# Optimization experiments

Hardware: AMD Instinct MI355X
Metric: run time of the kernel (lower is better)

## Reference

```python
import jax, jax.numpy as jnp
import numpy as np

N, D, H, E, K = 65536, 128, 256, 32, 2


def setup_inputs() -> dict:
    key = jax.random.key(0)
    ks = jax.random.split(key, 7)
    s_in = 1.0 / np.sqrt(D)
    s_hid = 1.0 / np.sqrt(H)
    return {
        "x": jax.random.normal(ks[0], (N, D), dtype=jnp.float32),
        "W1": jax.random.uniform(ks[1], (E, D, H), jnp.float32, -s_in, s_in),
        "b1": jax.random.uniform(ks[2], (E, H), jnp.float32, -s_in, s_in),
        "W2": jax.random.uniform(ks[3], (E, H, D), jnp.float32, -s_hid, s_hid),
        "b2": jax.random.uniform(ks[4], (E, D), jnp.float32, -s_hid, s_hid),
        "Wr": jax.random.uniform(ks[5], (D, E), jnp.float32, -s_in, s_in),
        "br": jax.random.uniform(ks[6], (E,), jnp.float32, -s_in, s_in),
    }


def reference(x, W1, b1, W2, b2, Wr, br):
    # Router (eval mode: no gate noise)
    logits = x @ Wr + br                                  # [N, E]
    scores = jax.nn.softmax(logits, axis=-1)              # [N, E]
    topk_vals, topk_inds = jax.lax.top_k(scores, K)       # [N, K]

    # dispatch_mask: zeros scattered with top-k probs (scatter_ on dim 1)
    n = x.shape[0]
    dispatch_mask = jnp.zeros_like(scores).at[
        jnp.arange(n)[:, None], topk_inds
    ].set(topk_vals)                                      # [N, E]

    # Dense all-experts compute, as in the reference torch.stack
    h = jax.nn.relu(jnp.einsum("nd,edh->neh", x, W1) + b1)   # [N, E, H]
    expert_outputs = jnp.einsum("neh,ehd->ned", h, W2) + b2  # [N, E, D]

    output = jnp.einsum("ned,ne->nd", expert_outputs, dispatch_mask)  # [N, D]

    importance = dispatch_mask.sum(axis=0)                # [E]
    imp_mean = jnp.mean(importance)
    imp_var = jnp.var(importance, ddof=1)                 # torch.var is unbiased
    load_balancing_loss = imp_var / (imp_mean ** 2 + 1e-9)
    return output, load_balancing_loss
```

## Files before the change

### kernel.cpp

```cpp
#include <hip/hip_runtime.h>
#include <hip/hip_bf16.h>
#include <cstdint>
#include <cstddef>

#define N_TOK 65536
#define DIM 128
#define HID 256
#define NE 32
#define TOPK 2

typedef __bf16 bf16x8 __attribute__((ext_vector_type(8)));
typedef float f32x4 __attribute__((ext_vector_type(4)));
typedef unsigned uint4v __attribute__((ext_vector_type(4)));

#define LDSA(c, row, byte) ((((c) * 1024 + (row) * 16 + (byte))) ^ ((((c) & 3) << 5)))

__device__ __forceinline__ unsigned short f2bf(float f) {
  unsigned u = __builtin_bit_cast(unsigned, f);
  u += 0x7fffu + ((u >> 16) & 1u);
  return (unsigned short)(u >> 16);
}
__device__ __forceinline__ float bf2f(unsigned s) {
  return __builtin_bit_cast(float, s << 16);
}
__device__ __forceinline__ uint2 split2(float f0, float f1) {
  unsigned u0 = __builtin_bit_cast(unsigned, f0);
  unsigned u1 = __builtin_bit_cast(unsigned, f1);
  unsigned hi = (u0 >> 16) | (u1 & 0xffff0000u);
  float r0 = f0 - __builtin_bit_cast(float, u0 & 0xffff0000u);
  float r1 = f1 - __builtin_bit_cast(float, u1 & 0xffff0000u);
  unsigned lo = (__builtin_bit_cast(unsigned, r0) >> 16) |
                (__builtin_bit_cast(unsigned, r1) & 0xffff0000u);
  uint2 ret; ret.x = hi; ret.y = lo;
  return ret;
}

__global__ void k_zero_out(float* __restrict__ out) {
  int t = blockIdx.x * 256 + threadIdx.x;
  float4 z = make_float4(0.f, 0.f, 0.f, 0.f);
  float4* o4 = (float4*)out;
  o4[t] = z;
  o4[t + 1048576] = z;
}

__global__ __launch_bounds__(256, 2) void k_front(
    const float* __restrict__ x, const float* __restrict__ W1,
    const float* __restrict__ W2, const float* __restrict__ Wr,
    const float* __restrict__ br,
    int* __restrict__ top_idx, float* __restrict__ top_val,
    unsigned short* __restrict__ xb,
    unsigned short* __restrict__ w1t, unsigned short* __restrict__ w2t,
    int* __restrict__ histbuf, float* __restrict__ impbuf) {
  int b = blockIdx.x;
  int t = threadIdx.x;

  if (b >= 512) {
    int bb = b - 512;
    const float* in;
    unsigned short* outp;
    int K, r0, c0;
    bool isW1;
    if (bb < 256) {
      int e = bb >> 3, tt = bb & 7;
      in = W1 + (size_t)e * DIM * HID;
      outp = w1t + (size_t)e * DIM * HID;
      K = HID;
      r0 = (tt >> 2) * 64; c0 = (tt & 3) * 64;
      isW1 = true;
    } else {
      bb -= 256;
      int e = bb >> 3, tt = bb & 7;
      in = W2 + (size_t)e * HID * DIM;
      outp = w2t + (size_t)e * HID * DIM;
      K = DIM;
      r0 = (tt >> 1) * 64; c0 = (tt & 1) * 64;
      isW1 = false;
    }
    __shared__ float tile[64][65];
    int r = t >> 2, cs = (t & 3) * 16;
    const float* src = in + (size_t)(r0 + r) * K + c0 + cs;
#pragma unroll
    for (int j = 0; j < 4; ++j) {
      float4 v = *(const float4*)(src + j * 4);
      tile[r][cs + j * 4 + 0] = v.x;
      tile[r][cs + j * 4 + 1] = v.y;
      tile[r][cs + j * 4 + 2] = v.z;
      tile[r][cs + j * 4 + 3] = v.w;
    }
    __syncthreads();
#pragma unroll
    for (int p = 0; p < 2; ++p) {
      int orow = p * 32 + (t >> 3);
      int oc8 = (t & 7) * 8;
      int rr = r0 + oc8;
      unsigned pk[4];
#pragma unroll
      for (int q = 0; q < 4; ++q) {
        unsigned lo = f2bf(tile[oc8 + 2 * q][orow]);
        unsigned hi = f2bf(tile[oc8 + 2 * q + 1][orow]);
        pk[q] = lo | (hi << 16);
      }
      uint4 u;
      u.x = pk[0]; u.y = pk[1]; u.z = pk[2]; u.w = pk[3];
      int h = c0 + orow;
      int hp = isW1 ? ((h & ~63) | ((h & 3) << 4) | ((h & 63) >> 2))
                    : ((h & ~31) | ((h & 1) << 4) | ((h & 31) >> 1));
      size_t addr = (size_t)(rr >> 5) * (K * 32) + (size_t)hp * 32 + (rr & 31);
      *(uint4*)(outp + addr) = u;
    }
    return;
  }

  __shared__ int hc[NE];
  __shared__ float hf[NE];
  __shared__ int slist[128];
  __shared__ int scount;
  if (t < NE) { hc[t] = 0; hf[t] = 0.f; }
  if (t == 0) scount = 0;
  __syncthreads();

  int w = t >> 6, l = t & 63, quad = l >> 4, l15 = l & 15;
  int tok0 = b * 128 + w * 32;

  bf16x8 bfr[2][2][4];
#pragma unroll
  for (int nt = 0; nt < 2; ++nt)
#pragma unroll
    for (int kc = 0; kc < 4; ++kc) {
      unsigned hiw[4], low[4];
#pragma unroll
      for (int jp = 0; jp < 4; ++jp) {
        int k0 = kc * 32 + quad * 8 + jp * 2;
        int e = nt * 16 + l15;
        float w0 = Wr[k0 * NE + e];
        float w1v = Wr[(k0 + 1) * NE + e];
        uint2 s = split2(w0, w1v);
        hiw[jp] = s.x; low[jp] = s.y;
      }
      uint4v h4, l4;
      h4[0] = hiw[0]; h4[1] = hiw[1]; h4[2] = hiw[2]; h4[3] = hiw[3];
      l4[0] = low[0]; l4[1] = low[1]; l4[2] = low[2]; l4[3] = low[3];
      bfr[0][nt][kc] = __builtin_bit_cast(bf16x8, h4);
      bfr[1][nt][kc] = __builtin_bit_cast(bf16x8, l4);
    }

  f32x4 acc[2][2];
#pragma unroll
  for (int a = 0; a < 2; ++a)
#pragma unroll
    for (int bb = 0; bb < 2; ++bb) {
      f32x4 z = {0.f, 0.f, 0.f, 0.f};
      acc[a][bb] = z;
    }

#pragma unroll
  for (int mt = 0; mt < 2; ++mt) {
    const float* xp = x + (size_t)(tok0 + mt * 16 + l15) * DIM + quad * 8;
    float4 va[4][2];
#pragma unroll
    for (int kc = 0; kc < 4; ++kc) {
      const float4* p = (const float4*)(xp + kc * 32);
      va[kc][0] = p[0];
      va[kc][1] = p[1];
    }
    unsigned short* xrow = xb + (size_t)(tok0 + mt * 16 + l15) * DIM + quad * 8;
#pragma unroll
    for (int kc = 0; kc < 4; ++kc) {
      uint4 u;
      u.x = (unsigned)f2bf(va[kc][0].x) | ((unsigned)f2bf(va[kc][0].y) << 16);
      u.y = (unsigned)f2bf(va[kc][0].z) | ((unsigned)f2bf(va[kc][0].w) << 16);
      u.z = (unsigned)f2bf(va[kc][1].x) | ((unsigned)f2bf(va[kc][1].y) << 16);
      u.w = (unsigned)f2bf(va[kc][1].z) | ((unsigned)f2bf(va[kc][1].w) << 16);
      *(uint4*)(xrow + kc * 32) = u;
    }
#pragma unroll
    for (int kc = 0; kc < 4; ++kc) {
      uint2 s0 = split2(va[kc][0].x, va[kc][0].y);
      uint2 s1 = split2(va[kc][0].z, va[kc][0].w);
      uint2 s2 = split2(va[kc][1].x, va[kc][1].y);
      uint2 s3 = split2(va[kc][1].z, va[kc][1].w);
      uint4v hu, lu;
      hu[0] = s0.x; lu[0] = s0.y;
      hu[1] = s1.x; lu[1] = s1.y;
      hu[2] = s2.x; lu[2] = s2.y;
      hu[3] = s3.x; lu[3] = s3.y;
      bf16x8 ahi = __builtin_bit_cast(bf16x8, hu);
      bf16x8 alo = __builtin_bit_cast(bf16x8, lu);
#pragma unroll
      for (int nt = 0; nt < 2; ++nt) {
        acc[mt][nt] = __builtin_amdgcn_mfma_f32_16x16x32_bf16(ahi, bfr[0][nt][kc], acc[mt][nt], 0, 0, 0);
        acc[mt][nt] = __builtin_amdgcn_mfma_f32_16x16x32_bf16(ahi, bfr[1][nt][kc], acc[mt][nt], 0, 0, 0);
        acc[mt][nt] = __builtin_amdgcn_mfma_f32_16x16x32_bf16(alo, bfr[0][nt][kc], acc[mt][nt], 0, 0, 0);
      }
    }
  }

  float brv0 = br[l15], brv1 = br[16 + l15];
  const float NINF = -3.0e38f;
#pragma unroll
  for (int mt = 0; mt < 2; ++mt) {
#pragma unroll
    for (int r = 0; r < 4; ++r) {
      float c0 = acc[mt][0][r] + brv0;
      float c1 = acc[mt][1][r] + brv1;
      float va = (c0 >= c1) ? c0 : c1;
      int ia = (c0 >= c1) ? l15 : 16 + l15;
#pragma unroll
      for (int off = 1; off < 16; off <<= 1) {
        float ov = __shfl_xor(va, off);
        int oi = __shfl_xor(ia, off);
        if (ov > va || (ov == va && oi < ia)) { va = ov; ia = oi; }
      }
      float v1 = va; int i1 = ia;
      float d0 = (i1 == l15) ? NINF : c0;
      float d1 = (i1 == 16 + l15) ? NINF : c1;
      float vb = (d0 >= d1) ? d0 : d1;
      int ib = (d0 >= d1) ? l15 : 16 + l15;
#pragma unroll
      for (int off = 1; off < 16; off <<= 1) {
        float ov = __shfl_xor(vb, off);
        int oi = __shfl_xor(ib, off);
        if (ov > vb || (ov == vb && oi < ib)) { vb = ov; ib = oi; }
      }
      float v2 = vb; int i2 = ib;
      float e0 = (i1 == l15 || i2 == l15) ? NINF : c0;
      float e1 = (i1 == 16 + l15 || i2 == 16 + l15) ? NINF : c1;
      float vc = (e0 >= e1) ? e0 : e1;
#pragma unroll
      for (int off = 1; off < 16; off <<= 1) {
        float ov = __shfl_xor(vc, off);
        vc = (ov > vc) ? ov : vc;
      }
      float s = __expf(c0 - v1) + __expf(c1 - v1);
#pragma unroll
      for (int off = 1; off < 16; off <<= 1) s += __shfl_xor(s, off);
      if (l15 == 0) {
        int n = tok0 + mt * 16 + quad * 4 + r;
        int2 ti; ti.x = i1; ti.y = i2;
        float2 tv; tv.x = 1.0f / s; tv.y = __expf(v2 - v1) / s;
        ((int2*)top_idx)[n] = ti;
        ((float2*)top_val)[n] = tv;
        atomicAdd(&hc[i1], 1);
        atomicAdd(&hc[i2], 1);
        atomicAdd(&hf[i1], tv.x);
        atomicAdd(&hf[i2], tv.y);
        if (v2 - vc < 2e-3f) {
          int si = atomicAdd(&scount, 1);
          if (si < 128) slist[si] = n;
        }
      }
    }
  }
  __syncthreads();

  int sc = scount;
  for (int s = (t >> 5); s < sc; s += 8) {
    int lt = t & 31;
    int n = slist[s];
    const float* xr = x + (size_t)n * DIM;
    double a = 0.0;
#pragma unroll 8
    for (int d = 0; d < DIM; ++d) a = fma((double)xr[d], (double)Wr[d * NE + lt], a);
    double lv = a + (double)br[lt];

    double v1 = lv; int i1 = lt;
#pragma unroll
    for (int off = 16; off > 0; off >>= 1) {
      double ov = __shfl_xor(v1, off, 32);
      int oi = __shfl_xor(i1, off, 32);
      if (ov > v1 || (ov == v1 && oi < i1)) { v1 = ov; i1 = oi; }
    }
    double lv2 = (lt == i1) ? -1.0e300 : lv;
    double v2 = lv2; int i2 = lt;
#pragma unroll
    for (int off = 16; off > 0; off >>= 1) {
      double ov = __shfl_xor(v2, off, 32);
      int oi = __shfl_xor(i2, off, 32);
      if (ov > v2 || (ov == v2 && oi < i2)) { v2 = ov; i2 = oi; }
    }
    float p = expf((float)(lv - v1));
    float ssum = p;
#pragma unroll
    for (int off = 16; off > 0; off >>= 1) ssum += __shfl_xor(ssum, off, 32);
    if (lt == 0) {
      int o1 = top_idx[n * 2 + 0];
      int o2 = top_idx[n * 2 + 1];
      float w1v = top_val[n * 2 + 0];
      float w2v = top_val[n * 2 + 1];
      float nv1 = 1.0f / ssum;
      float nv2 = expf((float)(v2 - v1)) / ssum;
      atomicAdd(&hc[o1], -1); atomicAdd(&hc[o2], -1);
      atomicAdd(&hc[i1], 1);  atomicAdd(&hc[i2], 1);
      atomicAdd(&hf[o1], -w1v); atomicAdd(&hf[o2], -w2v);
      atomicAdd(&hf[i1], nv1);  atomicAdd(&hf[i2], nv2);
      top_idx[n * 2 + 0] = i1;
      top_idx[n * 2 + 1] = i2;
      top_val[n * 2 + 0] = nv1;
      top_val[n * 2 + 1] = nv2;
    }
  }
  __syncthreads();
  if (t < NE) {
    histbuf[b * NE + t] = hc[t];
    impbuf[b * NE + t] = hf[t];
  }
}

__global__ __launch_bounds__(256) void k_scatter2(
    const int* __restrict__ top_idx, const float* __restrict__ top_val,
    const int* __restrict__ histbuf, const float* __restrict__ impbuf,
    int* __restrict__ perm, float* __restrict__ gatev, int* __restrict__ inv,
    int* __restrict__ offsets, int* __restrict__ counts, float* __restrict__ out_loss) {
  __shared__ int pf[8][32], pb[8][32];
  __shared__ int offs[NE], pref[NE], h2[NE];
  int b = blockIdx.x, t = threadIdx.x;
  if (t < NE) h2[t] = 0;
  int g = t >> 5, e = t & 31;
  int sf = 0, sb = 0;
  for (int j = 0; j < 64; ++j) {
    int bb = g * 64 + j;
    int v = histbuf[bb * NE + e];
    sf += v;
    sb += (bb < b) ? v : 0;
  }
  pf[g][e] = sf;
  pb[g][e] = sb;
  __syncthreads();
  if (t < 32) {
    int T = 0, P = 0;
#pragma unroll
    for (int g2 = 0; g2 < 8; ++g2) { T += pf[g2][t]; P += pb[g2][t]; }
    int pc = (T + 63) & ~63;
    int scn = pc;
#pragma unroll
    for (int off = 1; off < 32; off <<= 1) {
      int ov = __shfl_up(scn, off, 32);
      if (t >= off) scn += ov;
    }
    offs[t] = scn - pc;
    pref[t] = P;
    if (b == 0) {
      offsets[t] = scn - pc;
      counts[t] = T;
      if (t == 31) offsets[NE] = scn;
    }
  }
  __syncthreads();
  if (t < 128) {
    int n = b * 128 + t;
    int2 ti = ((const int2*)top_idx)[n];
    float2 tv = ((const float2*)top_val)[n];
    int r0 = atomicAdd(&h2[ti.x], 1);
    int r1 = atomicAdd(&h2[ti.y], 1);
    int p0 = offs[ti.x] + pref[ti.x] + r0;
    int p1 = offs[ti.y] + pref[ti.y] + r1;
    perm[p0] = n;
    gatev[p0] = tv.x;
    perm[p1] = n;
    gatev[p1] = tv.y;
    int2 iv; iv.x = p0; iv.y = p1;
    ((int2*)inv)[n] = iv;
  }
  if (b == 0) {
    __shared__ float pfi[8][32];
    float s2 = 0.f;
    for (int j = 0; j < 64; ++j) s2 += impbuf[(g * 64 + j) * NE + e];
    pfi[g][e] = s2;
    __syncthreads();
    if (t < 32) {
      float imp = 0.f;
#pragma unroll
      for (int g2 = 0; g2 < 8; ++g2) imp += pfi[g2][t];
      float ssum = imp;
#pragma unroll
      for (int off = 16; off > 0; off >>= 1) ssum += __shfl_xor(ssum, off, 32);
      float mean = ssum / 32.0f;
      float dlt = imp - mean;
      float v = dlt * dlt;
#pragma unroll
      for (int off = 16; off > 0; off >>= 1) v += __shfl_xor(v, off, 32);
      if (t == 0) *out_loss = (v / 31.0f) / (mean * mean + 1e-9f);
    }
  }
}

template <int YB>
__global__ __launch_bounds__(256, 3) void k_expert(
    const float* __restrict__ x, const unsigned short* __restrict__ xb,
    const unsigned short* __restrict__ w1t, const unsigned short* __restrict__ w2t,
    const float* __restrict__ b1, const float* __restrict__ b2,
    const int* __restrict__ offsets, const int* __restrict__ counts,
    const int* __restrict__ perm, const float* __restrict__ gatev,
    unsigned short* __restrict__ ybuf, float* __restrict__ out) {
  __shared__ __align__(16) unsigned char smem[32768];

  int bid = (int)(blockIdx.x & 7) * 260 + (int)(blockIdx.x >> 3);
  int slot0 = bid * 64;
  if (slot0 >= offsets[NE]) return;
  int e = 0;
#pragma unroll
  for (int i = 1; i < NE; ++i)
    if (slot0 >= offsets[i]) e = i;
  int cnt = counts[e];
  int local0 = slot0 - offsets[e];
  int nvalid = min(64, cnt - local0);

  int t = threadIdx.x;
  int w = t >> 6;
  int l = t & 63;
  int quad = l >> 4;
  int l15 = l & 15;

  int pvl = 0;
  float gvl = 0.f;
  if (YB) {
    uint4 v[4];
    if (l < nvalid) {
      pvl = perm[slot0 + l];
      gvl = gatev[slot0 + l];
      const uint4* rowp = (const uint4*)(xb + (size_t)pvl * DIM);
#pragma unroll
      for (int cc = 0; cc < 4; ++cc) v[cc] = rowp[w * 4 + cc];
    } else {
#pragma unroll
      for (int cc = 0; cc < 4; ++cc) { v[cc].x = 0u; v[cc].y = 0u; v[cc].z = 0u; v[cc].w = 0u; }
    }
#pragma unroll
    for (int cc = 0; cc < 4; ++cc)
      *(uint4*)(smem + LDSA(w * 4 + cc, l, 0)) = v[cc];
  } else {
    unsigned pk[16];
    if (l < nvalid) {
      pvl = perm[slot0 + l];
      gvl = gatev[slot0 + l];
      const float* src = x + (size_t)pvl * DIM + w * 32;
#pragma unroll
      for (int q = 0; q < 8; ++q) {
        float4 vv = ((const float4*)src)[q];
        pk[q * 2 + 0] = (unsigned)f2bf(vv.x) | ((unsigned)f2bf(vv.y) << 16);
        pk[q * 2 + 1] = (unsigned)f2bf(vv.z) | ((unsigned)f2bf(vv.w) << 16);
      }
    } else {
#pragma unroll
      for (int q = 0; q < 16; ++q) pk[q] = 0u;
    }
#pragma unroll
    for (int cc = 0; cc < 4; ++cc) {
      uint4 u;
      u.x = pk[cc * 4 + 0]; u.y = pk[cc * 4 + 1]; u.z = pk[cc * 4 + 2]; u.w = pk[cc * 4 + 3];
      *(uint4*)(smem + LDSA(w * 4 + cc, l, 0)) = u;
    }
  }

  const unsigned short* w1e = w1t + (size_t)e * DIM * HID;
  bf16x8 w1f[4][4];
#pragma unroll
  for (int kc = 0; kc < 4; ++kc)
#pragma unroll
    for (int jt = 0; jt < 4; ++jt)
      w1f[kc][jt] = *(const bf16x8*)(w1e + kc * 8192 + (w * 64 + jt * 16 + l15) * 32 + quad * 8);

  __syncthreads();

  f32x4 acc[4][4];
#pragma unroll
  for (int a = 0; a < 4; ++a)
#pragma unroll
    for (int bb = 0; bb < 4; ++bb) {
      f32x4 z = {0.f, 0.f, 0.f, 0.f};
      acc[a][bb] = z;
    }
#pragma unroll
  for (int kc = 0; kc < 4; ++kc) {
    bf16x8 af[4];
#pragma unroll
    for (int rt = 0; rt < 4; ++rt)
      af[rt] = *(const bf16x8*)(smem + LDSA(kc * 4 + quad, rt * 16 + l15, 0));
#pragma unroll
    for (int rt = 0; rt < 4; ++rt)
#pragma unroll
      for (int jt = 0; jt < 4; ++jt)
        acc[rt][jt] = __builtin_amdgcn_mfma_f32_16x16x32_bf16(af[rt], w1f[kc][jt], acc[rt][jt], 0, 0, 0);
  }

  const unsigned short* w2e = w2t + (size_t)e * HID * DIM;
  bf16x8 w2f[8][2];
#pragma unroll
  for (int hc = 0; hc < 8; ++hc)
#pragma unroll
    for (int jt = 0; jt < 2; ++jt)
      w2f[hc][jt] = *(const bf16x8*)(w2e + hc * 4096 + (w * 32 + jt * 16 + l15) * 32 + quad * 8);

  __syncthreads();

  {
    float4 b1v = *(const float4*)(b1 + e * HID + w * 64 + 4 * l15);
    int c = w * 8 + (l15 >> 1);
    int byte = (l15 & 1) * 8;
#pragma unroll
    for (int rt = 0; rt < 4; ++rt) {
#pragma unroll
      for (int r = 0; r < 4; ++r) {
        int tokrow = rt * 16 + quad * 4 + r;
        float v0 = acc[rt][0][r] + b1v.x; v0 = v0 > 0.f ? v0 : 0.f;
        float v1 = acc[rt][1][r] + b1v.y; v1 = v1 > 0.f ? v1 : 0.f;
        float v2 = acc[rt][2][r] + b1v.z; v2 = v2 > 0.f ? v2 : 0.f;
        float v3 = acc[rt][3][r] + b1v.w; v3 = v3 > 0.f ? v3 : 0.f;
        uint2 u;
        u.x = (unsigned)f2bf(v0) | ((unsigned)f2bf(v1) << 16);
        u.y = (unsigned)f2bf(v2) | ((unsigned)f2bf(v3) << 16);
        *(uint2*)(smem + LDSA(c, tokrow, byte)) = u;
      }
    }
  }
  __syncthreads();

  f32x4 accc[4][2];
#pragma unroll
  for (int a = 0; a < 4; ++a)
#pragma unroll
    for (int bb = 0; bb < 2; ++bb) {
      f32x4 z = {0.f, 0.f, 0.f, 0.f};
      accc[a][bb] = z;
    }
#pragma unroll
  for (int hc = 0; hc < 8; ++hc) {
    bf16x8 ah[4];
#pragma unroll
    for (int rt = 0; rt < 4; ++rt)
      ah[rt] = *(const bf16x8*)(smem + LDSA(hc * 4 + quad, rt * 16 + l15, 0));
#pragma unroll
    for (int rt = 0; rt < 4; ++rt)
#pragma unroll
      for (int jt = 0; jt < 2; ++jt)
        accc[rt][jt] = __builtin_amdgcn_mfma_f32_16x16x32_bf16(ah[rt], w2f[hc][jt], accc[rt][jt], 0, 0, 0);
  }

  int dbase = w * 32;
  float2 b2v = *(const float2*)(b2 + e * DIM + dbase + 2 * l15);
#pragma unroll
  for (int rt = 0; rt < 4; ++rt) {
#pragma unroll
    for (int r = 0; r < 4; ++r) {
      int tokrow = rt * 16 + quad * 4 + r;
      int pv = __shfl(pvl, tokrow);
      float g = __shfl(gvl, tokrow);
      if (tokrow < nvalid) {
        float y0 = g * (accc[rt][0][r] + b2v.x);
        float y1 = g * (accc[rt][1][r] + b2v.y);
        if (YB) {
          unsigned pack = (unsigned)f2bf(y0) | ((unsigned)f2bf(y1) << 16);
          *(unsigned*)(ybuf + (size_t)(slot0 + tokrow) * DIM + dbase + 2 * l15) = pack;
        } else {
          float* orow = out + (size_t)pv * DIM + dbase + 2 * l15;
          atomicAdd(&orow[0], y0);
          atomicAdd(&orow[1], y1);
        }
      }
    }
  }
}

__global__ __launch_bounds__(256) void k_combine(const unsigned short* __restrict__ ybuf,
                                                 const int* __restrict__ inv,
                                                 float* __restrict__ out) {
  int t = threadIdx.x;
  int n = blockIdx.x * 16 + (t >> 4);
  int lane = t & 15;
  int2 iv = ((const int2*)inv)[n];
  uint4 a = *((const uint4*)(ybuf + (size_t)iv.x * DIM) + lane);
  uint4 b = *((const uint4*)(ybuf + (size_t)iv.y * DIM) + lane);
  unsigned av[4] = {a.x, a.y, a.z, a.w}, bv[4] = {b.x, b.y, b.z, b.w};
  float r[8];
#pragma unroll
  for (int q = 0; q < 4; ++q) {
    r[q * 2 + 0] = bf2f(av[q] & 0xffffu) + bf2f(bv[q] & 0xffffu);
    r[q * 2 + 1] = bf2f(av[q] >> 16) + bf2f(bv[q] >> 16);
  }
  float* orow = out + (size_t)n * DIM + lane * 8;
  float4 w0 = {r[0], r[1], r[2], r[3]}, w1 = {r[4], r[5], r[6], r[7]};
  ((float4*)orow)[0] = w0;
  ((float4*)orow)[1] = w1;
}

extern "C" void kernel_launch(void* const* d_in, const int* in_sizes, int n_in,
                              void* d_out, int out_size, void* d_ws, size_t ws_size,
                              hipStream_t stream) {
  const float* x  = (const float*)d_in[0];
  const float* W1 = (const float*)d_in[1];
  const float* b1 = (const float*)d_in[2];
  const float* W2 = (const float*)d_in[3];
  const float* b2 = (const float*)d_in[4];
  const float* Wr = (const float*)d_in[5];
  const float* br = (const float*)d_in[6];
  float* out = (float*)d_out;

  char* ws = (char*)d_ws;
  int*   counts   = (int*)(ws + 0);
  int*   offsets  = (int*)(ws + 128);
  int*   top_idx  = (int*)(ws + 1024);
  float* top_val  = (float*)(ws + 525312);
  int*   perm     = (int*)(ws + 1049600);
  float* gatev    = (float*)(ws + 1582080);
  int*   inv      = (int*)(ws + 2114560);
  int*   histbuf  = (int*)(ws + 2638848);
  float* impbuf   = (float*)(ws + 2704384);
  unsigned short* w1t = (unsigned short*)(ws + 2769920);
  unsigned short* w2t = (unsigned short*)(ws + 4867072);
  unsigned short* ybuf = (unsigned short*)(ws + 6964224);
  const size_t NEEDED = 40518656;
  bool use_ybuf = ws_size >= NEEDED;

  unsigned short* xb = (unsigned short*)out;

  if (use_ybuf) {
    hipLaunchKernelGGL(k_front, dim3(1024), dim3(256), 0, stream, x, W1, W2, Wr, br,
                       top_idx, top_val, xb, w1t, w2t, histbuf, impbuf);
    hipLaunchKernelGGL(k_scatter2, dim3(512), dim3(256), 0, stream, top_idx, top_val,
                       histbuf, impbuf, perm, gatev, inv, offsets, counts,
                       out + (size_t)N_TOK * DIM);
    hipLaunchKernelGGL((k_expert<1>), dim3(2080), dim3(256), 0, stream, x, xb, w1t, w2t,
                       b1, b2, offsets, counts, perm, gatev, ybuf, out);
    hipLaunchKernelGGL(k_combine, dim3(4096), dim3(256), 0, stream, ybuf, inv, out);
  } else {
    hipLaunchKernelGGL(k_front, dim3(1024), dim3(256), 0, stream, x, W1, W2, Wr, br,
                       top_idx, top_val, xb, w1t, w2t, histbuf, impbuf);
    hipLaunchKernelGGL(k_scatter2, dim3(512), dim3(256), 0, stream, top_idx, top_val,
                       histbuf, impbuf, perm, gatev, inv, offsets, counts,
                       out + (size_t)N_TOK * DIM);
    hipLaunchKernelGGL(k_zero_out, dim3(4096), dim3(256), 0, stream, out);
    hipLaunchKernelGGL((k_expert<0>), dim3(2080), dim3(256), 0, stream, x,
                       (const unsigned short*)0, w1t, w2t, b1, b2, offsets, counts,
                       perm, gatev, (unsigned short*)0, out);
  }
}
```

Measured before the change: 178.0 us.

## Process two 64-token halves per expert block to reuse W1 fragments

Each expert block now handles 128 token slots as two 64-token halves. The W1 register fragments are loaded once and reused for both halves, and the second half's gather is issued early so it overlaps the first half's compute. W2 fragments are now streamed per hc iteration instead of held in registers, which frees registers but adds global loads inside the inner loop. Expert padding changes to 128, the grid halves, and the workspace is reordered so top_idx/top_val alias ybuf, adding extra padded rows and a longer serial chain per block.

```diff
diff --git a/kernel.cpp b/kernel.cpp
--- a/kernel.cpp
+++ b/kernel.cpp
@@ -330,7 +330,7 @@
     int T = 0, P = 0;
 #pragma unroll
     for (int g2 = 0; g2 < 8; ++g2) { T += pf[g2][t]; P += pb[g2][t]; }
-    int pc = (T + 63) & ~63;
+    int pc = (T + 127) & ~127;
     int scn = pc;
 #pragma unroll
     for (int off = 1; off < 32; off <<= 1) {
@@ -392,10 +392,11 @@
     const int* __restrict__ offsets, const int* __restrict__ counts,
     const int* __restrict__ perm, const float* __restrict__ gatev,
     unsigned short* __restrict__ ybuf, float* __restrict__ out) {
-  __shared__ __align__(16) unsigned char smem[32768];
-
-  int bid = (int)(blockIdx.x & 7) * 260 + (int)(blockIdx.x >> 3);
-  int slot0 = bid * 64;
+  __shared__ __align__(16) unsigned char xa[16384];
+  __shared__ __align__(16) unsigned char ha[32768];
+
+  int bid = (int)(blockIdx.x & 7) * 132 + (int)(blockIdx.x >> 3);
+  int slot0 = bid * 128;
   if (slot0 >= offsets[NE]) return;
   int e = 0;
 #pragma unroll
@@ -403,7 +404,9 @@
     if (slot0 >= offsets[i]) e = i;
   int cnt = counts[e];
   int local0 = slot0 - offsets[e];
-  int nvalid = min(64, cnt - local0);
+  int nvalid = min(128, cnt - local0);
+  int nv0 = nvalid < 64 ? nvalid : 64;
+  int nv1 = nvalid - nv0;
 
   int t = threadIdx.x;
   int w = t >> 6;
@@ -411,29 +414,40 @@
   int quad = l >> 4;
   int l15 = l & 15;
 
-  int pvl = 0;
-  float gvl = 0.f;
+  int pvl0 = 0, pvl1 = 0;
+  float gvl0 = 0.f, gvl1 = 0.f;
+  uint4 v1h[4];
   if (YB) {
-    uint4 v[4];
-    if (l < nvalid) {
-      pvl = perm[slot0 + l];
-      gvl = gatev[slot0 + l];
-      const uint4* rowp = (const uint4*)(xb + (size_t)pvl * DIM);
-#pragma unroll
-      for (int cc = 0; cc < 4; ++cc) v[cc] = rowp[w * 4 + cc];
+    uint4 v0[4];
+    if (l < nv0) {
+      pvl0 = perm[slot0 + l];
+      gvl0 = gatev[slot0 + l];
+      const uint4* rp = (const uint4*)(xb + (size_t)pvl0 * DIM);
+#pragma unroll
+      for (int cc = 0; cc < 4; ++cc) v0[cc] = rp[w * 4 + cc];
     } else {
 #pragma unroll
-      for (int cc = 0; cc < 4; ++cc) { v[cc].x = 0u; v[cc].y = 0u; v[cc].z = 0u; v[cc].w = 0u; }
+      for (int cc = 0; cc < 4; ++cc) { v0[cc].x = 0u; v0[cc].y = 0u; v0[cc].z = 0u; v0[cc].w = 0u; }
+    }
+    if (l < nv1) {
+      pvl1 = perm[slot0 + 64 + l];
+      gvl1 = gatev[slot0 + 64 + l];
+      const uint4* rp = (const uint4*)(xb + (size_t)pvl1 * DIM);
+#pragma unroll
+      for (int cc = 0; cc < 4; ++cc) v1h[cc] = rp[w * 4 + cc];
+    } else {
+#pragma unroll
+      for (int cc = 0; cc < 4; ++cc) { v1h[cc].x = 0u; v1h[cc].y = 0u; v1h[cc].z = 0u; v1h[cc].w = 0u; }
     }
 #pragma unroll
     for (int cc = 0; cc < 4; ++cc)
-      *(uint4*)(smem + LDSA(w * 4 + cc, l, 0)) = v[cc];
+      *(uint4*)(xa + LDSA(w * 4 + cc, l, 0)) = v0[cc];
   } else {
     unsigned pk[16];
-    if (l < nvalid) {
-      pvl = perm[slot0 + l];
-      gvl = gatev[slot0 + l];
-      const float* src = x + (size_t)pvl * DIM + w * 32;
+    if (l < nv0) {
+      pvl0 = perm[slot0 + l];
+      gvl0 = gatev[slot0 + l];
+      const float* src = x + (size_t)pvl0 * DIM + w * 32;
 #pragma unroll
       for (int q = 0; q < 8; ++q) {
         float4 vv = ((const float4*)src)[q];
@@ -444,11 +458,15 @@
 #pragma unroll
       for (int q = 0; q < 16; ++q) pk[q] = 0u;
     }
+    if (l < nv1) {
+      pvl1 = perm[slot0 + 64 + l];
+      gvl1 = gatev[slot0 + 64 + l];
+    }
 #pragma unroll
     for (int cc = 0; cc < 4; ++cc) {
       uint4 u;
       u.x = pk[cc * 4 + 0]; u.y = pk[cc * 4 + 1]; u.z = pk[cc * 4 + 2]; u.w = pk[cc * 4 + 3];
-      *(uint4*)(smem + LDSA(w * 4 + cc, l, 0)) = u;
+      *(uint4*)(xa + LDSA(w * 4 + cc, l, 0)) = u;
     }
   }
 
@@ -459,6 +477,11 @@
 #pragma unroll
     for (int jt = 0; jt < 4; ++jt)
       w1f[kc][jt] = *(const bf16x8*)(w1e + kc * 8192 + (w * 64 + jt * 16 + l15) * 32 + quad * 8);
+
+  const unsigned short* w2e = w2t + (size_t)e * HID * DIM;
+  float4 b1v = *(const float4*)(b1 + e * HID + w * 64 + 4 * l15);
+  int dbase = w * 32;
+  float2 b2v = *(const float2*)(b2 + e * DIM + dbase + 2 * l15);
 
   __syncthreads();
 
@@ -475,26 +498,42 @@
     bf16x8 af[4];
 #pragma unroll
     for (int rt = 0; rt < 4; ++rt)
-      af[rt] = *(const bf16x8*)(smem + LDSA(kc * 4 + quad, rt * 16 + l15, 0));
+      af[rt] = *(const bf16x8*)(xa + LDSA(kc * 4 + quad, rt * 16 + l15, 0));
 #pragma unroll
     for (int rt = 0; rt < 4; ++rt)
 #pragma unroll
       for (int jt = 0; jt < 4; ++jt)
         acc[rt][jt] = __builtin_amdgcn_mfma_f32_16x16x32_bf16(af[rt], w1f[kc][jt], acc[rt][jt], 0, 0, 0);
   }
-
-  const unsigned short* w2e = w2t + (size_t)e * HID * DIM;
-  bf16x8 w2f[8][2];
-#pragma unroll
-  for (int hc = 0; hc < 8; ++hc)
-#pragma unroll
-    for (int jt = 0; jt < 2; ++jt)
-      w2f[hc][jt] = *(const bf16x8*)(w2e + hc * 4096 + (w * 32 + jt * 16 + l15) * 32 + quad * 8);
-
-  __syncthreads();
+  __syncthreads();
+
+  if (YB) {
+#pragma unroll
+    for (int cc = 0; cc < 4; ++cc)
+      *(uint4*)(xa + LDSA(w * 4 + cc, l, 0)) = v1h[cc];
+  } else {
+    unsigned pk[16];
+    if (l < nv1) {
+      const float* src = x + (size_t)pvl1 * DIM + w * 32;
+#pragma unroll
+      for (int q = 0; q < 8; ++q) {
+        float4 vv = ((const float4*)src)[q];
+        pk[q * 2 + 0] = (unsigned)f2bf(vv.x) | ((unsigned)f2bf(vv.y) << 16);
+        pk[q * 2 + 1] = (unsigned)f2bf(vv.z) | ((unsigned)f2bf(vv.w) << 16);
+      }
+    } else {
+#pragma unroll
+      for (int q = 0; q < 16; ++q) pk[q] = 0u;
+    }
+#pragma unroll
+    for (int cc = 0; cc < 4; ++cc) {
+      uint4 u;
+      u.x = pk[cc * 4 + 0]; u.y = pk[cc * 4 + 1]; u.z = pk[cc * 4 + 2]; u.w = pk[cc * 4 + 3];
+      *(uint4*)(xa + LDSA(w * 4 + cc, l, 0)) = u;
+    }
+  }
 
   {
-    float4 b1v = *(const float4*)(b1 + e * HID + w * 64 + 4 * l15);
     int c = w * 8 + (l15 >> 1);
     int byte = (l15 & 1) * 8;
 #pragma unroll
@@ -509,7 +548,7 @@
         uint2 u;
         u.x = (unsigned)f2bf(v0) | ((unsigned)f2bf(v1) << 16);
         u.y = (unsigned)f2bf(v2) | ((unsigned)f2bf(v3) << 16);
-        *(uint2*)(smem + LDSA(c, tokrow, byte)) = u;
+        *(uint2*)(ha + LDSA(c, tokrow, byte)) = u;
       }
     }
   }
@@ -523,34 +562,118 @@
       f32x4 z = {0.f, 0.f, 0.f, 0.f};
       accc[a][bb] = z;
     }
-#pragma unroll
+#pragma unroll 2
   for (int hc = 0; hc < 8; ++hc) {
+    bf16x8 w2c0 = *(const bf16x8*)(w2e + hc * 4096 + (w * 32 + l15) * 32 + quad * 8);
+    bf16x8 w2c1 = *(const bf16x8*)(w2e + hc * 4096 + (w * 32 + 16 + l15) * 32 + quad * 8);
     bf16x8 ah[4];
 #pragma unroll
     for (int rt = 0; rt < 4; ++rt)
-      ah[rt] = *(const bf16x8*)(smem + LDSA(hc * 4 + quad, rt * 16 + l15, 0));
-#pragma unroll
-    for (int rt = 0; rt < 4; ++rt)
-#pragma unroll
-      for (int jt = 0; jt < 2; ++jt)
-        accc[rt][jt] = __builtin_amdgcn_mfma_f32_16x16x32_bf16(ah[rt], w2f[hc][jt], accc[rt][jt], 0, 0, 0);
-  }
-
-  int dbase = w * 32;
-  float2 b2v = *(const float2*)(b2 + e * DIM + dbase + 2 * l15);
+      ah[rt] = *(const bf16x8*)(ha + LDSA(hc * 4 + quad, rt * 16 + l15, 0));
+#pragma unroll
+    for (int rt = 0; rt < 4; ++rt) {
+      accc[rt][0] = __builtin_amdgcn_mfma_f32_16x16x32_bf16(ah[rt], w2c0, accc[rt][0], 0, 0, 0);
+      accc[rt][1] = __builtin_amdgcn_mfma_f32_16x16x32_bf16(ah[rt], w2c1, accc[rt][1], 0, 0, 0);
+    }
+  }
 #pragma unroll
   for (int rt = 0; rt < 4; ++rt) {
 #pragma unroll
     for (int r = 0; r < 4; ++r) {
       int tokrow = rt * 16 + quad * 4 + r;
-      int pv = __shfl(pvl, tokrow);
-      float g = __shfl(gvl, tokrow);
-      if (tokrow < nvalid) {
+      int pv = __shfl(pvl0, tokrow);
+      float g = __shfl(gvl0, tokrow);
+      if (tokrow < nv0) {
         float y0 = g * (accc[rt][0][r] + b2v.x);
         float y1 = g * (accc[rt][1][r] + b2v.y);
         if (YB) {
           unsigned pack = (unsigned)f2bf(y0) | ((unsigned)f2bf(y1) << 16);
           *(unsigned*)(ybuf + (size_t)(slot0 + tokrow) * DIM + dbase + 2 * l15) = pack;
+        } else {
+          float* orow = out + (size_t)pv * DIM + dbase + 2 * l15;
+          atomicAdd(&orow[0], y0);
+          atomicAdd(&orow[1], y1);
+        }
+      }
+    }
+  }
+
+#pragma unroll
+  for (int a = 0; a < 4; ++a)
+#pragma unroll
+    for (int bb = 0; bb < 4; ++bb) {
+      f32x4 z = {0.f, 0.f, 0.f, 0.f};
+      acc[a][bb] = z;
+    }
+#pragma unroll
+  for (int kc = 0; kc < 4; ++kc) {
+    bf16x8 af[4];
+#pragma unroll
+    for (int rt = 0; rt < 4; ++rt)
+      af[rt] = *(const bf16x8*)(xa + LDSA(kc * 4 + quad, rt * 16 + l15, 0));
+#pragma unroll
+    for (int rt = 0; rt < 4; ++rt)
+#pragma unroll
+      for (int jt = 0; jt < 4; ++jt)
+        acc[rt][jt] = __builtin_amdgcn_mfma_f32_16x16x32_bf16(af[rt], w1f[kc][jt], acc[rt][jt], 0, 0, 0);
+  }
+  __syncthreads();
+
+  {
+    int c = w * 8 + (l15 >> 1);
+    int byte = (l15 & 1) * 8;
+#pragma unroll
+    for (int rt = 0; rt < 4; ++rt) {
+#pragma unroll
+      for (int r = 0; r < 4; ++r) {
+        int tokrow = rt * 16 + quad * 4 + r;
+        float v0 = acc[rt][0][r] + b1v.x; v0 = v0 > 0.f ? v0 : 0.f;
+        float v1 = acc[rt][1][r] + b1v.y; v1 = v1 > 0.f ? v1 : 0.f;
+        float v2 = acc[rt][2][r] + b1v.z; v2 = v2 > 0.f ? v2 : 0.f;
+        float v3 = acc[rt][3][r] + b1v.w; v3 = v3 > 0.f ? v3 : 0.f;
+        uint2 u;
+        u.x = (unsigned)f2bf(v0) | ((unsigned)f2bf(v1) << 16);
+        u.y = (unsigned)f2bf(v2) | ((unsigned)f2bf(v3) << 16);
+        *(uint2*)(ha + LDSA(c, tokrow, byte)) = u;
+      }
+    }
+  }
+  __syncthreads();
+
+#pragma unroll
+  for (int a = 0; a < 4; ++a)
+#pragma unroll
+    for (int bb = 0; bb < 2; ++bb) {
+      f32x4 z = {0.f, 0.f, 0.f, 0.f};
+      accc[a][bb] = z;
+    }
+#pragma unroll 2
+  for (int hc = 0; hc < 8; ++hc) {
+    bf16x8 w2c0 = *(const bf16x8*)(w2e + hc * 4096 + (w * 32 + l15) * 32 + quad * 8);
+    bf16x8 w2c1 = *(const bf16x8*)(w2e + hc * 4096 + (w * 32 + 16 + l15) * 32 + quad * 8);
+    bf16x8 ah[4];
+#pragma unroll
+    for (int rt = 0; rt < 4; ++rt)
+      ah[rt] = *(const bf16x8*)(ha + LDSA(hc * 4 + quad, rt * 16 + l15, 0));
+#pragma unroll
+    for (int rt = 0; rt < 4; ++rt) {
+      accc[rt][0] = __builtin_amdgcn_mfma_f32_16x16x32_bf16(ah[rt], w2c0, accc[rt][0], 0, 0, 0);
+      accc[rt][1] = __builtin_amdgcn_mfma_f32_16x16x32_bf16(ah[rt], w2c1, accc[rt][1], 0, 0, 0);
+    }
+  }
+#pragma unroll
+  for (int rt = 0; rt < 4; ++rt) {
+#pragma unroll
+    for (int r = 0; r < 4; ++r) {
+      int tokrow = rt * 16 + quad * 4 + r;
+      int pv = __shfl(pvl1, tokrow);
+      float g = __shfl(gvl1, tokrow);
+      if (tokrow < nv1) {
+        float y0 = g * (accc[rt][0][r] + b2v.x);
+        float y1 = g * (accc[rt][1][r] + b2v.y);
+        if (YB) {
+          unsigned pack = (unsigned)f2bf(y0) | ((unsigned)f2bf(y1) << 16);
+          *(unsigned*)(ybuf + (size_t)(slot0 + 64 + tokrow) * DIM + dbase + 2 * l15) = pack;
         } else {
           float* orow = out + (size_t)pv * DIM + dbase + 2 * l15;
           atomicAdd(&orow[0], y0);
@@ -598,17 +721,17 @@
   char* ws = (char*)d_ws;
   int*   counts   = (int*)(ws + 0);
   int*   offsets  = (int*)(ws + 128);
-  int*   top_idx  = (int*)(ws + 1024);
-  float* top_val  = (float*)(ws + 525312);
-  int*   perm     = (int*)(ws + 1049600);
-  float* gatev    = (float*)(ws + 1582080);
-  int*   inv      = (int*)(ws + 2114560);
-  int*   histbuf  = (int*)(ws + 2638848);
-  float* impbuf   = (float*)(ws + 2704384);
-  unsigned short* w1t = (unsigned short*)(ws + 2769920);
-  unsigned short* w2t = (unsigned short*)(ws + 4867072);
-  unsigned short* ybuf = (unsigned short*)(ws + 6964224);
-  const size_t NEEDED = 40518656;
+  int*   perm     = (int*)(ws + 1024);
+  float* gatev    = (float*)(ws + 541696);
+  int*   inv      = (int*)(ws + 1082368);
+  int*   histbuf  = (int*)(ws + 1606656);
+  float* impbuf   = (float*)(ws + 1672192);
+  unsigned short* w1t = (unsigned short*)(ws + 1737728);
+  unsigned short* w2t = (unsigned short*)(ws + 3834880);
+  unsigned short* ybuf = (unsigned short*)(ws + 5932032);
+  int*   top_idx  = (int*)(ws + 5932032);
+  float* top_val  = (float*)(ws + 6456320);
+  const size_t NEEDED = 40535040;
   bool use_ybuf = ws_size >= NEEDED;
 
   unsigned short* xb = (unsigned short*)out;
@@ -619,7 +742,7 @@
     hipLaunchKernelGGL(k_scatter2, dim3(512), dim3(256), 0, stream, top_idx, top_val,
                        histbuf, impbuf, perm, gatev, inv, offsets, counts,
                        out + (size_t)N_TOK * DIM);
-    hipLaunchKernelGGL((k_expert<1>), dim3(2080), dim3(256), 0, stream, x, xb, w1t, w2t,
+    hipLaunchKernelGGL((k_expert<1>), dim3(1056), dim3(256), 0, stream, x, xb, w1t, w2t,
                        b1, b2, offsets, counts, perm, gatev, ybuf, out);
     hipLaunchKernelGGL(k_combine, dim3(4096), dim3(256), 0, stream, ybuf, inv, out);
   } else {
@@ -629,7 +752,7 @@
                        histbuf, impbuf, perm, gatev, inv, offsets, counts,
                        out + (size_t)N_TOK * DIM);
     hipLaunchKernelGGL(k_zero_out, dim3(4096), dim3(256), 0, stream, out);
-    hipLaunchKernelGGL((k_expert<0>), dim3(2080), dim3(256), 0, stream, x,
+    hipLaunchKernelGGL((k_expert<0>), dim3(1056), dim3(256), 0, stream, x,
                        (const unsigned short*)0, w1t, w2t, b1, b2, offsets, counts,
                        perm, gatev, (unsigned short*)0, out);
   }
```

Result: slower. 207.7 us (+16.7%).
